# Kernel optimization log

Hardware: AMD Instinct MI355X
Metric: run time of the kernel (lower is better)

Reference implementation:

```python
import jax, jax.numpy as jnp
import numpy as np
from jax import lax

EPS = 1e-5
KH = KW = 3
K = KH * KW


def conv3x3(x, w, b=None):
    # x: [B,Cin,H,W], w: [Cout,Cin,3,3], padding=1, stride=1
    y = lax.conv_general_dilated(x, w, (1, 1), [(1, 1), (1, 1)],
                                 dimension_numbers=("NCHW", "OIHW", "NCHW"))
    if b is not None:
        y = y + b[None, :, None, None]
    return y


def deform_conv2d(x, offset, mask, weight):
    # torchvision-style deform_conv2d v2: kernel 3x3, stride 1, pad 1, dilation 1,
    # groups=1, offset_groups=1. offset: [B,2K,H,W] (dy,dx per tap), mask: [B,K,H,W].
    B, C, H, W = x.shape
    off = offset.reshape(B, K, 2, H, W)
    kidx = jnp.arange(K)
    kdy = (kidx // KW - 1).astype(x.dtype)[None, :, None, None]  # [1,K,1,1]
    kdx = (kidx % KW - 1).astype(x.dtype)[None, :, None, None]
    yy = jnp.arange(H, dtype=x.dtype)[None, None, :, None]
    xx = jnp.arange(W, dtype=x.dtype)[None, None, None, :]
    py = yy + kdy + off[:, :, 0]  # [B,K,H,W] sampling rows
    px = xx + kdx + off[:, :, 1]  # [B,K,H,W] sampling cols

    y0 = jnp.floor(py).astype(jnp.int32)
    x0 = jnp.floor(px).astype(jnp.int32)
    wy = py - y0.astype(x.dtype)
    wx = px - x0.astype(x.dtype)

    def gather_b(xb, yc, xc):
        # xb: [C,H,W]; yc, xc: [K,H,W] -> [C,K,H,W], zeros outside image
        valid = (yc >= 0) & (yc < H) & (xc >= 0) & (xc < W)
        v = xb[:, jnp.clip(yc, 0, H - 1), jnp.clip(xc, 0, W - 1)]
        return v * valid[None].astype(xb.dtype)

    gather = jax.vmap(gather_b, in_axes=(0, 0, 0))  # over batch

    w00 = ((1 - wy) * (1 - wx))[:, None]  # [B,1,K,H,W]
    w01 = ((1 - wy) * wx)[:, None]
    w10 = (wy * (1 - wx))[:, None]
    w11 = (wy * wx)[:, None]

    sampled = (gather(x, y0, x0) * w00 + gather(x, y0, x0 + 1) * w01 +
               gather(x, y0 + 1, x0) * w10 + gather(x, y0 + 1, x0 + 1) * w11)
    sampled = sampled * mask[:, None]  # [B,C,K,H,W]
    wk = weight.reshape(weight.shape[0], weight.shape[1], K)
    return jnp.einsum("bckhw,ock->bohw", sampled, wk)


def reference(f1_feat, f3_feat, offset_w, offset_b, main_w, gamma, beta):
    concat = jnp.concatenate([f1_feat, f3_feat], axis=1)
    om = conv3x3(concat, offset_w, offset_b)  # [B,27,H,W]
    offset = om[:, :18]
    mask = jax.nn.sigmoid(om[:, 18:])
    aligned = deform_conv2d(f1_feat, offset, mask, main_w)
    # BatchNorm2d, training mode (batch statistics, biased variance)
    mean = aligned.mean(axis=(0, 2, 3))
    var = aligned.var(axis=(0, 2, 3))
    xn = (aligned - mean[None, :, None, None]) * lax.rsqrt(var + EPS)[None, :, None, None]
    return xn * gamma[None, :, None, None] + beta[None, :, None, None]


def setup_inputs() -> dict:
    key = jax.random.key(0)
    ks = jax.random.split(key, 5)
    B, C, H, W = 4, 64, 128, 128
    f1 = jax.random.normal(ks[0], (B, C, H, W), jnp.float32)
    f3 = jax.random.normal(ks[1], (B, C, H, W), jnp.float32)
    # small offset-conv init so predicted offsets stay in-image (like trained nets)
    offset_w = jax.random.normal(ks[2], (27, 2 * C, 3, 3), jnp.float32) * 0.01
    offset_b = jnp.zeros((27,), jnp.float32)
    main_w = jax.random.normal(ks[3], (C, C, 3, 3), jnp.float32) * (1.0 / np.sqrt(C * 9))
    gamma = jnp.ones((C,), jnp.float32)
    beta = jnp.zeros((C,), jnp.float32)
    return {"f1_feat": f1, "f3_feat": f3, "offset_w": offset_w,
            "offset_b": offset_b, "main_w": main_w, "gamma": gamma, "beta": beta}
```

## Files before the change

### kernel.cpp

```cpp
#include <hip/hip_runtime.h>
#include <math.h>

#define BB 4
#define CC 64
#define HH 128
#define WW 128
#define HWP 16384

typedef _Float16 h2 __attribute__((ext_vector_type(2)));
typedef _Float16 h4 __attribute__((ext_vector_type(4)));
typedef __fp16  p2 __attribute__((ext_vector_type(2)));
typedef float f32x4 __attribute__((ext_vector_type(4)));
union HU { unsigned u; h2 h; p2 p; };
union U2H { uint2 u; h4 h; };
static __device__ __forceinline__ h2 u2h(unsigned x){ HU v; v.u = x; return v.h; }
static __device__ __forceinline__ unsigned h2u(h2 x){ HU v; v.h = x; return v.u; }
static __device__ __forceinline__ unsigned pk2u(float a, float b){
    HU v; v.p = __builtin_amdgcn_cvt_pkrtz(a, b); return v.u;
}

__global__ __launch_bounds__(256) void kTm(
    const float* __restrict__ f1, const float* __restrict__ f3,
    const float* __restrict__ ow, const float* __restrict__ mw,
    unsigned* __restrict__ f13t, unsigned* __restrict__ wmf,
    unsigned* __restrict__ wof)
{
    __shared__ float lt[64*129];
    int t = threadIdx.x;
    if (blockIdx.x < 512) {
        int b = blockIdx.x >> 7, y = blockIdx.x & 127;
        unsigned* dst = f13t + ((size_t)((b << 14) + (y << 7)))*64;
        for (int half = 0; half < 2; ++half) {
            const float* src = (half == 0 ? f1 : f3) + (((size_t)b*64) << 14) + (y << 7);
#pragma unroll 4
            for (int i = 0; i < 32; ++i) {
                int idx = i*256 + t; int c = idx >> 7, x = idx & 127;
                lt[c*129 + x] = src[(c << 14) + x];
            }
            __syncthreads();
#pragma unroll 4
            for (int i = 0; i < 16; ++i) {
                int idx = i*256 + t; int x = idx >> 5, cp = idx & 31;
                dst[x*64 + half*32 + cp] = pk2u(lt[(2*cp)*129 + x], lt[(2*cp+1)*129 + x]);
            }
            __syncthreads();
        }
        return;
    }
    int i = (blockIdx.x - 512)*256 + t;
    if (i < 18432) {
        int j   = i & 1;
        int t2  = i >> 1;
        int kb  = t2 % 36;
        int rl  = t2 / 36;
        int l   = rl & 63;
        int r   = rl >> 6;
        int row = l & 15, ksel = l >> 4;
        int och = r*16 + row;
        int P   = kb*8 + ksel*2 + j;
        int kt  = P >> 5;
        int cp  = P & 31;
        float lo = mw[och*576 + (2*cp    )*9 + kt];
        float hi = mw[och*576 + (2*cp + 1)*9 + kt];
        wmf[i] = pk2u(lo, hi);
    } else if (i < 36864) {
        int idx = i - 18432;
        int j   = idx & 1;
        int t2  = idx >> 1;
        int kb  = t2 % 72;
        int rl  = t2 / 72;
        int l   = rl & 63;
        int mt  = rl >> 6;
        int row = l & 15, ksel = l >> 4;
        int och = mt*16 + row;
        int P   = kb*8 + ksel*2 + j;
        int kt  = P >> 6;
        int cp  = P & 63;
        unsigned v = 0;
        if (och < 27) {
            float lo = ow[(och*128 + 2*cp    )*9 + kt];
            float hi = ow[(och*128 + 2*cp + 1)*9 + kt];
            v = pk2u(lo, hi);
        }
        wof[idx] = v;
    }
}

__global__ __launch_bounds__(256) void k1_offset_conv(
    const unsigned* __restrict__ f13t, const unsigned* __restrict__ wof,
    const float* __restrict__ ob, float* __restrict__ om)
{
    extern __shared__ unsigned tile[];

    int blk0 = blockIdx.x;
    int blk  = ((blk0 & 7) << 7) | (blk0 >> 3);
    int xq = blk & 3;
    int yp = (blk >> 2) & 63;
    int b  = blk >> 8;
    int y0r = yp << 1;

    int tid  = threadIdx.x;
    int lane = tid & 63;
    int wv   = tid >> 6;
    int mt   = wv >> 1;
    int ys   = wv & 1;
    int row  = lane & 15;
    int ksel = lane >> 4;

#pragma unroll 1
    for (int s = 0; s < 4; ++s) {
        int yy = y0r + s - 1;
        bool yok = (unsigned)yy < (unsigned)HH;
        unsigned* ts = tile + s*2312;
        for (int i = tid; i < 544; i += 256) {
            int px34 = i >> 4, q = i & 15;
            int gxp = xq*32 - 1 + px34;
            uint4 v = make_uint4(0u, 0u, 0u, 0u);
            if (yok && (unsigned)gxp < (unsigned)WW)
                v = *(const uint4*)&f13t[(((size_t)(b*128 + yy))*128 + gxp)*64 + q*4];
            *(uint4*)&ts[px34*68 + q*4] = v;
        }
    }
    __syncthreads();

    f32x4 acc0 = {0.f, 0.f, 0.f, 0.f};
    f32x4 acc1 = {0.f, 0.f, 0.f, 0.f};
    const unsigned* wbase = wof + (size_t)(mt*64 + lane)*144;

#pragma unroll 1
    for (int dy = 0; dy < 3; ++dy) {
        const unsigned* ts = tile + (ys + dy)*2312;
#pragma unroll
        for (int hf = 0; hf < 2; ++hf) {
            uint4 wq[6];
#pragma unroll
            for (int m = 0; m < 6; ++m)
                wq[m] = *(const uint4*)&wbase[dy*48 + hf*24 + m*4];
#pragma unroll
            for (int kl = 0; kl < 12; ++kl) {
                int Pl  = (hf*12 + kl)*8 + ksel*2;
                int ktl = Pl >> 6;
                int cp  = Pl & 63;
                U2H wa;
                uint4 q = wq[kl >> 1];
                if (kl & 1) { wa.u.x = q.z; wa.u.y = q.w; }
                else        { wa.u.x = q.x; wa.u.y = q.y; }
                U2H b0, b1;
                b0.u = *(const uint2*)&ts[(row + ktl)*68 + cp];
                b1.u = *(const uint2*)&ts[(16 + row + ktl)*68 + cp];
                acc0 = __builtin_amdgcn_mfma_f32_16x16x16f16(wa.h, b0.h, acc0, 0, 0, 0);
                acc1 = __builtin_amdgcn_mfma_f32_16x16x16f16(wa.h, b1.h, acc1, 0, 0, 0);
            }
        }
    }

    int y  = y0r + ys;
    int gx0 = xq*32 + row;
#pragma unroll
    for (int rI = 0; rI < 4; ++rI) {
        int och = mt*16 + ksel*4 + rI;
        if (och < 27) {
            float v0 = acc0[rI] + ob[och];
            float v1 = acc1[rI] + ob[och];
            if (och >= 18) {
                v0 = 1.f / (1.f + __expf(-v0));
                v1 = 1.f / (1.f + __expf(-v1));
            }
            int base = ((b*27 + och) << 14) + (y << 7) + gx0;
            om[base]      = v0;
            om[base + 16] = v1;
        }
    }
}

__global__ __launch_bounds__(256) void k2_deform(
    const unsigned* __restrict__ f13t, const unsigned* __restrict__ wmf,
    const float* __restrict__ om, unsigned* __restrict__ alignedh,
    float* __restrict__ part)
{
    extern __shared__ unsigned lds[];
    unsigned* pl_a = lds;
    unsigned* pl_w = lds + 576;
    unsigned* sl   = lds + 1728;

    int blk0 = blockIdx.x;
    int blk  = ((blk0 & 7) << 7) | (blk0 >> 3);
    int xh = blk & 1;
    int y  = (blk >> 1) & 127;
    int b  = blk >> 8;

    int tid  = threadIdx.x;
    int lane = tid & 63;
    int wv   = tid >> 6;
    int row  = lane & 15;
    int ksel = lane >> 4;
    int cg   = tid & 7;
    int grp  = tid >> 3;
    int pwb  = ((cg >> 2) << 4) | ((cg & 1) << 3) | (((cg >> 1) & 1) << 1);

    const float* omb = om + ((b*27) << 14) + (y << 7);
    const unsigned* ftb = f13t + (((size_t)b) << 20);

    for (int i = tid; i < 576; i += 256) {
        int k = i >> 6, lpx = i & 63;
        int gxp = xh*64 + lpx;
        float off0 = omb[((2*k)   << 14) + gxp];
        float off1 = omb[((2*k+1) << 14) + gxp];
        float mk   = omb[((18+k)  << 14) + gxp];

        float pyf = (float)y   + (float)(k/3) - 1.f + off0;
        float pxg = (float)gxp + (float)(k%3) - 1.f + off1;
        float fy = floorf(pyf), fx = floorf(pxg);
        int y0 = (int)fy, x0 = (int)fx;
        float wy = pyf - fy, wx = pxg - fx;
        float oy = 1.f - wy, ox = 1.f - wx;
        bool yv0 = (unsigned)y0     < (unsigned)HH;
        bool yv1 = (unsigned)(y0+1) < (unsigned)HH;
        bool xv0 = (unsigned)x0     < (unsigned)WW;
        bool xv1 = (unsigned)(x0+1) < (unsigned)WW;
        int y0c = min(max(y0, 0), 127);
        int x0c = min(max(x0, 0), 127);
        int dy = min(max(y0+1, 0), 127) - y0c;
        int dx = min(max(x0+1, 0), 127) - x0c;
        unsigned a = (unsigned)((y0c << 7) + x0c) | ((unsigned)dx << 14) | ((unsigned)dy << 15);
        float w00 = (yv0 && xv0) ? oy*ox*mk : 0.f;
        float w01 = (yv0 && xv1) ? oy*wx*mk : 0.f;
        float w10 = (yv1 && xv0) ? wy*ox*mk : 0.f;
        float w11 = (yv1 && xv1) ? wy*wx*mk : 0.f;
        pl_a[i] = a;
        pl_w[i*2]     = pk2u(w00, w01);
        pl_w[i*2 + 1] = pk2u(w10, w11);
    }
    __syncthreads();

    f32x4 accA = {0.f,0.f,0.f,0.f};
    f32x4 accB = {0.f,0.f,0.f,0.f};
    f32x4 accC = {0.f,0.f,0.f,0.f};
    f32x4 accD = {0.f,0.f,0.f,0.f};

    const unsigned* wbase = wmf + (wv*64 + lane)*72;

#pragma unroll 1
    for (int th = 0; th < 3; ++th) {
        uint4 wq[6];
#pragma unroll
        for (int m = 0; m < 6; ++m)
            wq[m] = *(const uint4*)&wbase[th*24 + m*4];

#pragma unroll 3
        for (int it = 0; it < 6; ++it) {
            int item = it*32 + grp;
            int ktl  = item >> 6;
            int px   = item & 63;
            int k    = th*3 + ktl;
            int pidx = k*64 + px;
            unsigned a = pl_a[pidx];
            uint2 wpk = *(const uint2*)&pl_w[pidx*2];
            int i00 = (int)(a & 0x3FFFu);
            int dx  = (int)((a >> 14) & 1u);
            int i10 = i00 + (((int)(a >> 15) & 1) << 7);
            h2 hw01 = u2h(wpk.x);
            h2 hw23 = u2h(wpk.y);
            h2 w00d = {hw01.x, hw01.x}, w01d = {hw01.y, hw01.y};
            h2 w10d = {hw23.x, hw23.x}, w11d = {hw23.y, hw23.y};

            uint4 t00 = *(const uint4*)&ftb[(size_t)(i00     )*64 + 4*cg];
            uint4 t01 = *(const uint4*)&ftb[(size_t)(i00 + dx)*64 + 4*cg];
            uint4 t10 = *(const uint4*)&ftb[(size_t)(i10     )*64 + 4*cg];
            uint4 t11 = *(const uint4*)&ftb[(size_t)(i10 + dx)*64 + 4*cg];

            h2 v0 = u2h(t00.x)*w00d + u2h(t01.x)*w01d + u2h(t10.x)*w10d + u2h(t11.x)*w11d;
            h2 v1 = u2h(t00.y)*w00d + u2h(t01.y)*w01d + u2h(t10.y)*w10d + u2h(t11.y)*w11d;
            h2 v2 = u2h(t00.z)*w00d + u2h(t01.z)*w01d + u2h(t10.z)*w10d + u2h(t11.z)*w11d;
            h2 v3 = u2h(t00.w)*w00d + u2h(t01.w)*w01d + u2h(t10.w)*w10d + u2h(t11.w)*w11d;

            int bs = px*100 + ktl*32 + pwb;
            *(uint2*)&sl[bs]     = make_uint2(h2u(v0), h2u(v1));
            *(uint2*)&sl[bs + 4] = make_uint2(h2u(v2), h2u(v3));
        }
        __syncthreads();

        const unsigned* bpA = &sl[(row     )*100 + ksel*4];
        const unsigned* bpB = &sl[(16+row  )*100 + ksel*4];
        const unsigned* bpC = &sl[(32+row  )*100 + ksel*4];
        const unsigned* bpD = &sl[(48+row  )*100 + ksel*4];
#pragma unroll
        for (int m = 0; m < 6; ++m) {
            uint4 bvA = *(const uint4*)&bpA[m*16];
            uint4 bvB = *(const uint4*)&bpB[m*16];
            uint4 bvC = *(const uint4*)&bpC[m*16];
            uint4 bvD = *(const uint4*)&bpD[m*16];
            U2H waA, waB, sa, sb;
            waA.u.x = wq[m].x; waA.u.y = wq[m].y;
            waB.u.x = wq[m].z; waB.u.y = wq[m].w;
            sa.u.x = bvA.x; sa.u.y = bvA.y;
            sb.u.x = bvA.z; sb.u.y = bvA.w;
            accA = __builtin_amdgcn_mfma_f32_16x16x16f16(waA.h, sa.h, accA, 0, 0, 0);
            accA = __builtin_amdgcn_mfma_f32_16x16x16f16(waB.h, sb.h, accA, 0, 0, 0);
            sa.u.x = bvB.x; sa.u.y = bvB.y;
            sb.u.x = bvB.z; sb.u.y = bvB.w;
            accB = __builtin_amdgcn_mfma_f32_16x16x16f16(waA.h, sa.h, accB, 0, 0, 0);
            accB = __builtin_amdgcn_mfma_f32_16x16x16f16(waB.h, sb.h, accB, 0, 0, 0);
            sa.u.x = bvC.x; sa.u.y = bvC.y;
            sb.u.x = bvC.z; sb.u.y = bvC.w;
            accC = __builtin_amdgcn_mfma_f32_16x16x16f16(waA.h, sa.h, accC, 0, 0, 0);
            accC = __builtin_amdgcn_mfma_f32_16x16x16f16(waB.h, sb.h, accC, 0, 0, 0);
            sa.u.x = bvD.x; sa.u.y = bvD.y;
            sb.u.x = bvD.z; sb.u.y = bvD.w;
            accD = __builtin_amdgcn_mfma_f32_16x16x16f16(waA.h, sa.h, accD, 0, 0, 0);
            accD = __builtin_amdgcn_mfma_f32_16x16x16f16(waB.h, sb.h, accD, 0, 0, 0);
        }
        __syncthreads();
    }

    float* sred = (float*)lds;
#pragma unroll
    for (int rI = 0; rI < 4; ++rI) {
        int och = wv*16 + ksel*4 + rI;
        float v0 = accA[rI], v1 = accB[rI], v2 = accC[rI], v3 = accD[rI];
        int ai = (((b*CC + och) << 13)) + (y << 6) + row;
        alignedh[ai + ((2*xh    ) << 4)] = pk2u(v0, v1);
        alignedh[ai + ((2*xh + 1) << 4)] = pk2u(v2, v3);
        float s  = v0 + v1 + v2 + v3;
        float sq = v0*v0 + v1*v1 + v2*v2 + v3*v3;
#pragma unroll
        for (int off = 1; off < 16; off <<= 1) {
            s  += __shfl_xor(s,  off, 64);
            sq += __shfl_xor(sq, off, 64);
        }
        if (row == 0) { sred[och] = s; sred[64 + och] = sq; }
    }
    __syncthreads();
    for (int i = tid; i < 128; i += 256)
        part[(size_t)blk*128 + i] = sred[i];
}

__global__ __launch_bounds__(256) void k3b_reduce(
    const float* __restrict__ part, float* __restrict__ stats)
{
    int i = blockIdx.x;
    int tid = threadIdx.x;
    float s = 0.f;
    for (int j = tid; j < 1024; j += 256) s += part[(size_t)j*128 + i];
    for (int off = 32; off > 0; off >>= 1) s += __shfl_down(s, off, 64);
    __shared__ float rs[4];
    int w = tid >> 6;
    if ((tid & 63) == 0) rs[w] = s;
    __syncthreads();
    if (tid == 0) stats[i] = rs[0] + rs[1] + rs[2] + rs[3];
}

__global__ __launch_bounds__(256) void k4_norm(
    const unsigned* __restrict__ alignedh, const float* __restrict__ stats,
    const float* __restrict__ gamma, const float* __restrict__ beta,
    float* __restrict__ out)
{
    const float invN = 1.f / 65536.f;
    int i4 = blockIdx.x*256 + threadIdx.x;
    int u  = i4 << 2;
    int c  = (u >> 13) & 63;
    int lx = u & 15;
    int xq = (u >> 4) & 3;
    int y  = (u >> 6) & 127;
    int bc = u >> 13;

    float mean = stats[c] * invN;
    float var  = stats[64 + c] * invN - mean*mean;
    float sc = gamma[c] * rsqrtf(var + 1e-5f);
    float sh = beta[c] - mean*sc;

    uint4 v = *(const uint4*)&alignedh[u];
    h2 p0 = u2h(v.x), p1 = u2h(v.y), p2 = u2h(v.z), p3 = u2h(v.w);
    float4 lo = make_float4((float)p0.x*sc + sh, (float)p1.x*sc + sh,
                            (float)p2.x*sc + sh, (float)p3.x*sc + sh);
    float4 hi = make_float4((float)p0.y*sc + sh, (float)p1.y*sc + sh,
                            (float)p2.y*sc + sh, (float)p3.y*sc + sh);
    int ob = (bc << 14) + (y << 7) + xq*32 + lx;
    *(float4*)&out[ob]      = lo;
    *(float4*)&out[ob + 16] = hi;
}

extern "C" void kernel_launch(void* const* d_in, const int* in_sizes, int n_in,
                              void* d_out, int out_size, void* d_ws, size_t ws_size,
                              hipStream_t stream)
{
    const float* f1    = (const float*)d_in[0];
    const float* f3    = (const float*)d_in[1];
    const float* ow    = (const float*)d_in[2];
    const float* ob    = (const float*)d_in[3];
    const float* mw    = (const float*)d_in[4];
    const float* gamma = (const float*)d_in[5];
    const float* beta  = (const float*)d_in[6];
    float* out = (float*)d_out;

    float* om     = (float*)d_ws;
    float* stats  = om + 4*27*HWP;
    unsigned* wmf = (unsigned*)(stats + 512);
    unsigned* wof = wmf + 18432;
    unsigned* f13t = wof + 18432;
    float* part   = (float*)(f13t + 4*HWP*64);
    unsigned* alignedh = (unsigned*)(part + 2048*128);

    const int lds1 = 4*2312*4;
    const int lds2 = (1728 + 64*100) * 4;
    (void)hipFuncSetAttribute((const void*)k1_offset_conv,
        hipFuncAttributeMaxDynamicSharedMemorySize, lds1);
    (void)hipFuncSetAttribute((const void*)k2_deform,
        hipFuncAttributeMaxDynamicSharedMemorySize, lds2);

    hipLaunchKernelGGL(kTm, dim3(656), dim3(256), 0, stream,
                       f1, f3, ow, mw, f13t, wmf, wof);
    hipLaunchKernelGGL(k1_offset_conv, dim3(1024), dim3(256), lds1, stream,
                       f13t, wof, ob, om);
    hipLaunchKernelGGL(k2_deform, dim3(1024), dim3(256), lds2, stream,
                       f13t, wmf, om, alignedh, part);
    hipLaunchKernelGGL(k3b_reduce, dim3(128), dim3(256), 0, stream, part, stats);
    hipLaunchKernelGGL(k4_norm, dim3(2048), dim3(256), 0, stream,
                       alignedh, stats, gamma, beta, out);
}
```

Measured before the change: 63.19 us.

## Double deform kernel block to 512 threads, splitting pixel halves across waves

```diff
diff --git a/kernel.cpp b/kernel.cpp
--- a/kernel.cpp
+++ b/kernel.cpp
@@ -173,7 +173,7 @@
     }
 }
 
-__global__ __launch_bounds__(256) void k2_deform(
+__global__ __launch_bounds__(512) void k2_deform(
     const unsigned* __restrict__ f13t, const unsigned* __restrict__ wmf,
     const float* __restrict__ om, unsigned* __restrict__ alignedh,
     float* __restrict__ part)
@@ -192,8 +192,10 @@
     int tid  = threadIdx.x;
     int lane = tid & 63;
     int wv   = tid >> 6;
+    int ot   = wv & 3;
+    int ph   = wv >> 2;
     int row  = lane & 15;
-    int ksel = lane >> 4;
+    int ksel = (lane >> 4) & 3;
     int cg   = tid & 7;
     int grp  = tid >> 3;
     int pwb  = ((cg >> 2) << 4) | ((cg & 1) << 3) | (((cg >> 1) & 1) << 1);
@@ -201,7 +203,7 @@
     const float* omb = om + ((b*27) << 14) + (y << 7);
     const unsigned* ftb = f13t + (((size_t)b) << 20);
 
-    for (int i = tid; i < 576; i += 256) {
+    for (int i = tid; i < 576; i += 512) {
         int k = i >> 6, lpx = i & 63;
         int gxp = xh*64 + lpx;
         float off0 = omb[((2*k)   << 14) + gxp];
@@ -235,10 +237,8 @@
 
     f32x4 accA = {0.f,0.f,0.f,0.f};
     f32x4 accB = {0.f,0.f,0.f,0.f};
-    f32x4 accC = {0.f,0.f,0.f,0.f};
-    f32x4 accD = {0.f,0.f,0.f,0.f};
-
-    const unsigned* wbase = wmf + (wv*64 + lane)*72;
+
+    const unsigned* wbase = wmf + (ot*64 + lane)*72;
 
 #pragma unroll 1
     for (int th = 0; th < 3; ++th) {
@@ -247,9 +247,9 @@
         for (int m = 0; m < 6; ++m)
             wq[m] = *(const uint4*)&wbase[th*24 + m*4];
 
-#pragma unroll 3
-        for (int it = 0; it < 6; ++it) {
-            int item = it*32 + grp;
+#pragma unroll
+        for (int it = 0; it < 3; ++it) {
+            int item = it*64 + grp;
             int ktl  = item >> 6;
             int px   = item & 63;
             int k    = th*3 + ktl;
@@ -280,16 +280,12 @@
         }
         __syncthreads();
 
-        const unsigned* bpA = &sl[(row     )*100 + ksel*4];
-        const unsigned* bpB = &sl[(16+row  )*100 + ksel*4];
-        const unsigned* bpC = &sl[(32+row  )*100 + ksel*4];
-        const unsigned* bpD = &sl[(48+row  )*100 + ksel*4];
+        const unsigned* bpA = &sl[(32*ph + row     )*100 + ksel*4];
+        const unsigned* bpB = &sl[(32*ph + 16 + row)*100 + ksel*4];
 #pragma unroll
         for (int m = 0; m < 6; ++m) {
             uint4 bvA = *(const uint4*)&bpA[m*16];
             uint4 bvB = *(const uint4*)&bpB[m*16];
-            uint4 bvC = *(const uint4*)&bpC[m*16];
-            uint4 bvD = *(const uint4*)&bpD[m*16];
             U2H waA, waB, sa, sb;
             waA.u.x = wq[m].x; waA.u.y = wq[m].y;
             waB.u.x = wq[m].z; waB.u.y = wq[m].w;
@@ -301,14 +297,6 @@
             sb.u.x = bvB.z; sb.u.y = bvB.w;
             accB = __builtin_amdgcn_mfma_f32_16x16x16f16(waA.h, sa.h, accB, 0, 0, 0);
             accB = __builtin_amdgcn_mfma_f32_16x16x16f16(waB.h, sb.h, accB, 0, 0, 0);
-            sa.u.x = bvC.x; sa.u.y = bvC.y;
-            sb.u.x = bvC.z; sb.u.y = bvC.w;
-            accC = __builtin_amdgcn_mfma_f32_16x16x16f16(waA.h, sa.h, accC, 0, 0, 0);
-            accC = __builtin_amdgcn_mfma_f32_16x16x16f16(waB.h, sb.h, accC, 0, 0, 0);
-            sa.u.x = bvD.x; sa.u.y = bvD.y;
-            sb.u.x = bvD.z; sb.u.y = bvD.w;
-            accD = __builtin_amdgcn_mfma_f32_16x16x16f16(waA.h, sa.h, accD, 0, 0, 0);
-            accD = __builtin_amdgcn_mfma_f32_16x16x16f16(waB.h, sb.h, accD, 0, 0, 0);
         }
         __syncthreads();
     }
@@ -316,23 +304,25 @@
     float* sred = (float*)lds;
 #pragma unroll
     for (int rI = 0; rI < 4; ++rI) {
-        int och = wv*16 + ksel*4 + rI;
-        float v0 = accA[rI], v1 = accB[rI], v2 = accC[rI], v3 = accD[rI];
+        int och = ot*16 + ksel*4 + rI;
+        float v0 = accA[rI], v1 = accB[rI];
         int ai = (((b*CC + och) << 13)) + (y << 6) + row;
-        alignedh[ai + ((2*xh    ) << 4)] = pk2u(v0, v1);
-        alignedh[ai + ((2*xh + 1) << 4)] = pk2u(v2, v3);
-        float s  = v0 + v1 + v2 + v3;
-        float sq = v0*v0 + v1*v1 + v2*v2 + v3*v3;
+        alignedh[ai + ((2*xh + ph) << 4)] = pk2u(v0, v1);
+        float s  = v0 + v1;
+        float sq = v0*v0 + v1*v1;
 #pragma unroll
         for (int off = 1; off < 16; off <<= 1) {
             s  += __shfl_xor(s,  off, 64);
             sq += __shfl_xor(sq, off, 64);
         }
-        if (row == 0) { sred[och] = s; sred[64 + och] = sq; }
+        if (row == 0) {
+            sred[ph*128 + och]      = s;
+            sred[ph*128 + 64 + och] = sq;
+        }
     }
     __syncthreads();
-    for (int i = tid; i < 128; i += 256)
-        part[(size_t)blk*128 + i] = sred[i];
+    for (int i = tid; i < 128; i += 512)
+        part[(size_t)blk*128 + i] = sred[i] + sred[128 + i];
 }
 
 __global__ __launch_bounds__(256) void k3b_reduce(
@@ -412,7 +402,7 @@
                        f1, f3, ow, mw, f13t, wmf, wof);
     hipLaunchKernelGGL(k1_offset_conv, dim3(1024), dim3(256), lds1, stream,
                        f13t, wof, ob, om);
-    hipLaunchKernelGGL(k2_deform, dim3(1024), dim3(256), lds2, stream,
+    hipLaunchKernelGGL(k2_deform, dim3(1024), dim3(512), lds2, stream,
                        f13t, wmf, om, alignedh, part);
     hipLaunchKernelGGL(k3b_reduce, dim3(128), dim3(256), 0, stream, part, stats);
     hipLaunchKernelGGL(k4_norm, dim3(2048), dim3(256), 0, stream,
```

Result: slower. 72.69 us (+15.0%).
